# Kernel optimization log

Hardware: AMD Instinct MI355X
Metric: run time of the kernel (lower is better)

## Reference

```python
import jax, jax.numpy as jnp
import numpy as np

B, N, F_IN, H1, H2 = 32, 1024, 512, 256, 128


def _leaky(x, alpha):
    return jnp.where(x >= 0, x, alpha * x)


def _gat_layer(x, W, a, alpha=0.01, concat=True):
    # x: [B,N,Fin], W: [Fin,Fout], a: [2*Fout,1]
    h = x @ W                              # [B,N,Fout]
    Fo = W.shape[1]
    # The repeat+cat+matmul(a) in torch is exactly a_left . h_i + a_right . h_j
    el = h @ a[:Fo, 0]                     # [B,N]
    er = h @ a[Fo:, 0]                     # [B,N]
    e = _leaky(el[:, :, None] + er[:, None, :], alpha)   # [B,N,N]
    # global per-batch min-max normalization, then *30 - 20
    mn = jnp.min(e, axis=(1, 2), keepdims=True)
    mx = jnp.max(e, axis=(1, 2), keepdims=True)
    e = (e - mn) / (mx - mn) * 30.0 - 20.0
    att = jax.nn.sigmoid(e)                # [B,N,N]; dropout is a no-op in eval
    hp = att @ h                           # [B,N,Fout]
    if concat:
        hp = jax.nn.elu(hp)
    return hp, att


def setup_inputs() -> dict:
    key = jax.random.key(0)
    ks = jax.random.split(key, 8)
    x = jax.random.normal(ks[0], (B, N, F_IN), dtype=jnp.float32)
    edge_weight = jax.random.normal(ks[1], (B, N, N), dtype=jnp.float32)
    def xavier(k, shape):
        fan_in, fan_out = shape[0], shape[1]
        lim = 1.414 * np.sqrt(6.0 / (fan_in + fan_out))
        return jax.random.uniform(k, shape, jnp.float32, -lim, lim)
    W1 = xavier(ks[2], (F_IN, H1))
    a1 = xavier(ks[3], (2 * H1, 1))
    W2 = xavier(ks[4], (H1, H2))
    a2 = xavier(ks[5], (2 * H2, 1))
    Wg = jax.random.normal(ks[6], (H2, 1), dtype=jnp.float32) * np.sqrt(2.0 / H2)
    bg = jnp.zeros((1,), dtype=jnp.float32)
    return {"x": x, "edge_weight": edge_weight, "W1": W1, "a1": a1,
            "W2": W2, "a2": a2, "Wg": Wg, "bg": bg}


def reference(x, edge_weight, W1, a1, W2, a2, Wg, bg):
    # edge_weight ('adj') is never used inside GraphAttentionLayer.forward
    g1, fc1 = _gat_layer(x, W1, a1, alpha=0.01, concat=True)
    g2, fc2 = _gat_layer(g1, W2, a2, alpha=0.01, concat=False)
    # VanillaGCN: leaky_relu(BN(Linear(adj @ feats))); BN is identity in eval
    z = (fc2 @ g2) @ Wg + bg               # [B,N,1]
    out = _leaky(z, 0.01)
    return out, fc2, g2
```

## Files before the change

kernel.cpp:

```cpp
#include <hip/hip_runtime.h>

#define NN 1024
#define FIN 512
#define HH1 256
#define HH2 128
#define MTOT 32768

typedef unsigned short ushort_t;
using bf16x8 = __attribute__((ext_vector_type(8))) short;
using f32x4  = __attribute__((ext_vector_type(4))) float;

__device__ __forceinline__ float leakyf(float x) { return fmaxf(x, 0.01f * x); }
__device__ __forceinline__ float eluf(float x) { return x > 0.0f ? x : __expf(x) - 1.0f; }
__device__ __forceinline__ unsigned pack_hi(unsigned u0, unsigned u1) {
  return __builtin_amdgcn_perm(u1, u0, 0x07060302u);
}
__device__ __forceinline__ void split_pack2(float f0, float f1, unsigned& hp, unsigned& lp) {
  unsigned u0 = __float_as_uint(f0), u1 = __float_as_uint(f1);
  hp = pack_hi(u0, u1);
  float l0 = f0 - __uint_as_float(u0 & 0xFFFF0000u);
  float l1 = f1 - __uint_as_float(u1 & 0xFFFF0000u);
  lp = pack_hi(__float_as_uint(l0), __float_as_uint(l1));
}
__device__ __forceinline__ unsigned pack_rne(float f0, float f1) {
  unsigned u0 = __float_as_uint(f0); u0 += 0x7FFFu + ((u0 >> 16) & 1u);
  unsigned u1 = __float_as_uint(f1); u1 += 0x7FFFu + ((u1 >> 16) & 1u);
  return pack_hi(u0, u1);
}

__global__ __launch_bounds__(256) void transpose_w_split(const float* __restrict__ W,
                                                         ushort_t* __restrict__ WThi,
                                                         ushort_t* __restrict__ WTlo,
                                                         int Nc, int kshift) {
  int idx = blockIdx.x * 256 + threadIdx.x;
  int k = idx & ((1 << kshift) - 1);
  int n = idx >> kshift;
  float f = W[(size_t)k * Nc + n];
  unsigned u = __float_as_uint(f);
  WThi[idx] = (ushort_t)(u >> 16);
  float lo = f - __uint_as_float(u & 0xFFFF0000u);
  WTlo[idx] = (ushort_t)(__float_as_uint(lo) >> 16);
}

template<int NC>
__global__ __launch_bounds__(256) void gemm_asplit(const float* __restrict__ A,
                                                   const ushort_t* __restrict__ BThi,
                                                   const ushort_t* __restrict__ BTlo,
                                                   const float* __restrict__ avec,
                                                   ushort_t* __restrict__ CThi,
                                                   ushort_t* __restrict__ CTlo,
                                                   float* __restrict__ el,
                                                   float* __restrict__ er, int K) {
  constexpr int NFR = NC / 32;
  constexpr int NB  = NC / 64;
  __shared__ ushort_t Ah[64 * 40], Al[64 * 40];
  __shared__ ushort_t Bbuf[NC * 80];
  __shared__ float aL[NC], aR[NC];
  ushort_t* Bh = Bbuf;
  ushort_t* Bl = Bbuf + NC * 40;
  const int t = threadIdx.x, lane = t & 63, wid = t >> 6;
  const int wm = (wid & 1) * 32, wn = (wid >> 1) * (NC / 2);
  const int ln = lane & 15, quad = lane >> 4;
  const int m0 = blockIdx.x * 64;
  if (t < NC) { aL[t] = avec[t]; aR[t] = avec[NC + t]; }
  const int ra = t >> 2, ka = (t & 3) * 8;
  const float* ap = A + (size_t)(m0 + ra) * K + ka;
  const int brow = (t >> 2);
  const int bko  = (t & 3) * 8;
  f32x4 acc[2][NFR];
#pragma unroll
  for (int mi = 0; mi < 2; ++mi)
#pragma unroll
    for (int ni = 0; ni < NFR; ++ni) acc[mi][ni] = (f32x4){0.f, 0.f, 0.f, 0.f};

  for (int k0 = 0; k0 < K; k0 += 32) {
    float4 fa0 = *(const float4*)(ap + k0);
    float4 fa1 = *(const float4*)(ap + k0 + 4);
    uint4 vbh[NB], vbl[NB];
#pragma unroll
    for (int i = 0; i < NB; ++i) {
      size_t off = (size_t)(brow + i * 64) * K + k0 + bko;
      vbh[i] = *(const uint4*)&BThi[off];
      vbl[i] = *(const uint4*)&BTlo[off];
    }
    uint4 ah4, al4;
    split_pack2(fa0.x, fa0.y, ah4.x, al4.x);
    split_pack2(fa0.z, fa0.w, ah4.y, al4.y);
    split_pack2(fa1.x, fa1.y, ah4.z, al4.z);
    split_pack2(fa1.z, fa1.w, ah4.w, al4.w);
    __syncthreads();
    *(uint4*)&Ah[ra * 40 + ka] = ah4;
    *(uint4*)&Al[ra * 40 + ka] = al4;
#pragma unroll
    for (int i = 0; i < NB; ++i) {
      *(uint4*)&Bh[(brow + i * 64) * 40 + bko] = vbh[i];
      *(uint4*)&Bl[(brow + i * 64) * 40 + bko] = vbl[i];
    }
    __syncthreads();
    bf16x8 ahf[2], alf[2], bhf[NFR], blf[NFR];
#pragma unroll
    for (int i = 0; i < 2; ++i) {
      const int ao = (wm + i * 16 + ln) * 40 + quad * 8;
      ahf[i] = *(const bf16x8*)&Ah[ao];
      alf[i] = *(const bf16x8*)&Al[ao];
    }
#pragma unroll
    for (int i = 0; i < NFR; ++i) {
      const int bo = (wn + i * 16 + ln) * 40 + quad * 8;
      bhf[i] = *(const bf16x8*)&Bh[bo];
      blf[i] = *(const bf16x8*)&Bl[bo];
    }
#pragma unroll
    for (int mi = 0; mi < 2; ++mi)
#pragma unroll
      for (int ni = 0; ni < NFR; ++ni) {
        acc[mi][ni] = __builtin_amdgcn_mfma_f32_16x16x32_bf16(ahf[mi], bhf[ni], acc[mi][ni], 0, 0, 0);
        acc[mi][ni] = __builtin_amdgcn_mfma_f32_16x16x32_bf16(ahf[mi], blf[ni], acc[mi][ni], 0, 0, 0);
        acc[mi][ni] = __builtin_amdgcn_mfma_f32_16x16x32_bf16(alf[mi], bhf[ni], acc[mi][ni], 0, 0, 0);
      }
  }

#pragma unroll
  for (int mi = 0; mi < 2; ++mi) {
    const int mr = m0 + wm + mi * 16 + quad * 4;
#pragma unroll
    for (int rr = 0; rr < 4; ++rr) {
      float vel = 0.f, ver = 0.f;
#pragma unroll
      for (int ni = 0; ni < NFR; ++ni) {
        const int c = wn + ni * 16 + ln;
        vel = fmaf(acc[mi][ni][rr], aL[c], vel);
        ver = fmaf(acc[mi][ni][rr], aR[c], ver);
      }
#pragma unroll
      for (int m = 1; m < 16; m <<= 1) {
        vel += __shfl_xor(vel, m);
        ver += __shfl_xor(ver, m);
      }
      if (ln == 0) {
        atomicAdd(&el[mr + rr], vel);
        atomicAdd(&er[mr + rr], ver);
      }
    }
  }

  ushort_t* dsthi = CThi + (size_t)blockIdx.x * (NC * 64);
  ushort_t* dstlo = CTlo + (size_t)blockIdx.x * (NC * 64);
  const int colbase = wid * (NC / 4);
  const int g = lane >> 2, j = lane & 3;
#pragma unroll
  for (int pass = 0; pass < 2; ++pass) {
    __syncthreads();
#pragma unroll
    for (int mi = 0; mi < 2; ++mi) {
      const int rbase = wm + mi * 16 + quad * 4;
#pragma unroll
      for (int ni = 0; ni < NFR; ++ni) {
        const int c = wn + ni * 16 + ln;
        unsigned h01, l01, h23, l23;
        split_pack2(acc[mi][ni][0], acc[mi][ni][1], h01, l01);
        split_pack2(acc[mi][ni][2], acc[mi][ni][3], h23, l23);
        uint2 v = pass ? make_uint2(l01, l23) : make_uint2(h01, h23);
        *(uint2*)&Bbuf[c * 66 + rbase] = v;
      }
    }
    __syncthreads();
    ushort_t* dst = pass ? dstlo : dsthi;
#pragma unroll
    for (int cc = 0; cc < NC / 64; ++cc) {
      const int col = colbase + cc * 16 + g;
#pragma unroll
      for (int half = 0; half < 2; ++half) {
        const int r = half * 32 + j * 8;
        *(uint4*)&dst[col * 64 + r] = *(const uint4*)&Bbuf[col * 66 + r];
      }
    }
  }
}

__global__ __launch_bounds__(256) void minmax_params(const float* __restrict__ el,
                                                     const float* __restrict__ er,
                                                     float2* __restrict__ params) {
  __shared__ float smnl[256], smxl[256], smnr[256], smxr[256];
  const int b = blockIdx.x, t = threadIdx.x;
  float mnl = 3.4e38f, mxl = -3.4e38f, mnr = 3.4e38f, mxr = -3.4e38f;
  for (int i = t; i < NN; i += 256) {
    float v = el[b * NN + i];
    mnl = fminf(mnl, v); mxl = fmaxf(mxl, v);
    float u = er[b * NN + i];
    mnr = fminf(mnr, u); mxr = fmaxf(mxr, u);
  }
  smnl[t] = mnl; smxl[t] = mxl; smnr[t] = mnr; smxr[t] = mxr;
  __syncthreads();
  for (int s = 128; s > 0; s >>= 1) {
    if (t < s) {
      smnl[t] = fminf(smnl[t], smnl[t + s]);
      smxl[t] = fmaxf(smxl[t], smxl[t + s]);
      smnr[t] = fminf(smnr[t], smnr[t + s]);
      smxr[t] = fmaxf(smxr[t], smxr[t + s]);
    }
    __syncthreads();
  }
  if (t == 0) {
    float mn = leakyf(smnl[0] + smnr[0]);
    float mx = leakyf(smxl[0] + smxr[0]);
    params[b] = make_float2(mn, 30.0f / (mx - mn));
  }
}

__global__ __launch_bounds__(256) void gemm_att2(const float* __restrict__ el,
                                                 const float* __restrict__ er,
                                                 const float2* __restrict__ params,
                                                 const ushort_t* __restrict__ hThi,
                                                 const ushort_t* __restrict__ hTlo,
                                                 float* __restrict__ C,
                                                 const float* __restrict__ wg,
                                                 float* __restrict__ wv,
                                                 int Nc, int doElu) {
  __shared__ ushort_t Ah[64 * 40];
  __shared__ ushort_t Bh[128 * 40], Bl[128 * 40];
  __shared__ float ers[NN];
  __shared__ float wls[128];
  const int b = blockIdx.z, t = threadIdx.x, lane = t & 63, wid = t >> 6;
  const int wm = (wid & 1) * 32, wn = (wid >> 1) * 64;
  const int ln = lane & 15, quad = lane >> 4;
  const int m0 = blockIdx.x * 64, n0 = blockIdx.y * 128;
  const float2 p = params[b];
  const float npinv = -p.y;
  const float npc   = p.x * p.y + 20.0f;
  *(float4*)&ers[t * 4] = *(const float4*)&er[b * NN + t * 4];
  if (wg && t < 128) wls[t] = wg[t];
  const int ra = t >> 2, ka = (t & 3) * 8;
  const float elv = el[b * NN + m0 + ra];
  const int rb = t >> 1, kb = (t & 1) * 16;
  const size_t tstride = (size_t)Nc * 64;
  const size_t rowoff  = (size_t)(n0 + rb) * 64 + kb;
  f32x4 acc[2][4];
#pragma unroll
  for (int mi = 0; mi < 2; ++mi)
#pragma unroll
    for (int ni = 0; ni < 4; ++ni) acc[mi][ni] = (f32x4){0.f, 0.f, 0.f, 0.f};
  __syncthreads();

  for (int k0 = 0; k0 < NN; k0 += 32) {
    const size_t toff = (size_t)(b * 16 + (k0 >> 6)) * tstride + (size_t)(k0 & 32) + rowoff;
    uint4 vbh0 = *(const uint4*)&hThi[toff];
    uint4 vbh1 = *(const uint4*)&hThi[toff + 8];
    uint4 vbl0 = *(const uint4*)&hTlo[toff];
    uint4 vbl1 = *(const uint4*)&hTlo[toff + 8];
    float s[8];
#pragma unroll
    for (int j = 0; j < 8; ++j) {
      float x = elv + ers[k0 + ka + j];
      x = fmaxf(x, 0.01f * x);
      s[j] = __builtin_amdgcn_rcpf(1.0f + __expf(fmaf(x, npinv, npc)));
    }
    uint4 av;
    av.x = pack_rne(s[0], s[1]); av.y = pack_rne(s[2], s[3]);
    av.z = pack_rne(s[4], s[5]); av.w = pack_rne(s[6], s[7]);
    __syncthreads();
    *(uint4*)&Ah[ra * 40 + ka] = av;
    *(uint4*)&Bh[rb * 40 + kb] = vbh0; *(uint4*)&Bh[rb * 40 + kb + 8] = vbh1;
    *(uint4*)&Bl[rb * 40 + kb] = vbl0; *(uint4*)&Bl[rb * 40 + kb + 8] = vbl1;
    __syncthreads();
    bf16x8 af[2], bhf[4], blf[4];
#pragma unroll
    for (int i = 0; i < 2; ++i) af[i] = *(const bf16x8*)&Ah[(wm + i * 16 + ln) * 40 + quad * 8];
#pragma unroll
    for (int i = 0; i < 4; ++i) {
      const int bo = (wn + i * 16 + ln) * 40 + quad * 8;
      bhf[i] = *(const bf16x8*)&Bh[bo];
      blf[i] = *(const bf16x8*)&Bl[bo];
    }
#pragma unroll
    for (int mi = 0; mi < 2; ++mi)
#pragma unroll
      for (int ni = 0; ni < 4; ++ni) {
        acc[mi][ni] = __builtin_amdgcn_mfma_f32_16x16x32_bf16(af[mi], bhf[ni], acc[mi][ni], 0, 0, 0);
        acc[mi][ni] = __builtin_amdgcn_mfma_f32_16x16x32_bf16(af[mi], blf[ni], acc[mi][ni], 0, 0, 0);
      }
  }
#pragma unroll
  for (int mi = 0; mi < 2; ++mi) {
    const int mrl = m0 + wm + mi * 16 + quad * 4;
    const size_t mrow = (size_t)b * NN + mrl;
#pragma unroll
    for (int ni = 0; ni < 4; ++ni) {
      const int c = n0 + wn + ni * 16 + ln;
#pragma unroll
      for (int rr = 0; rr < 4; ++rr) {
        float v = acc[mi][ni][rr];
        if (doElu) v = eluf(v);
        C[(mrow + rr) * Nc + c] = v;
      }
    }
    if (wg) {
#pragma unroll
      for (int rr = 0; rr < 4; ++rr) {
        float vw = 0.f;
#pragma unroll
        for (int ni = 0; ni < 4; ++ni)
          vw = fmaf(acc[mi][ni][rr], wls[wn + ni * 16 + ln], vw);
#pragma unroll
        for (int m = 1; m < 16; m <<= 1) vw += __shfl_xor(vw, m);
        if (ln == 0) atomicAdd(&wv[b * NN + mrl + rr], vw);
      }
    }
  }
}

__global__ __launch_bounds__(256) void final_out_fc2(const float* __restrict__ el,
                                                     const float* __restrict__ er,
                                                     const float2* __restrict__ params,
                                                     const float* __restrict__ w,
                                                     const float* __restrict__ bg,
                                                     float* __restrict__ fc2,
                                                     float* __restrict__ out) {
  const int row  = (blockIdx.x * 256 + threadIdx.x) >> 6;
  const int lane = threadIdx.x & 63;
  const int b = row >> 10;
  const float2 p = params[b];
  const float npinv = -p.y;
  const float npc   = p.x * p.y + 20.0f;
  const float eli = el[row];
  const float* erb = er + (b << 10);
  const float* wb  = w + (b << 10);
  float* fcrow = fc2 + (size_t)row * NN;
  float s = 0.f;
  for (int j = lane * 4; j < NN; j += 256) {
    float4 e4 = *(const float4*)&erb[j];
    float4 w4 = *(const float4*)&wb[j];
    float4 a;
    a.x = __builtin_amdgcn_rcpf(1.0f + __expf(fmaf(leakyf(eli + e4.x), npinv, npc)));
    a.y = __builtin_amdgcn_rcpf(1.0f + __expf(fmaf(leakyf(eli + e4.y), npinv, npc)));
    a.z = __builtin_amdgcn_rcpf(1.0f + __expf(fmaf(leakyf(eli + e4.z), npinv, npc)));
    a.w = __builtin_amdgcn_rcpf(1.0f + __expf(fmaf(leakyf(eli + e4.w), npinv, npc)));
    s += w4.x * a.x + w4.y * a.y + w4.z * a.z + w4.w * a.w;
    *(float4*)&fcrow[j] = a;
  }
#pragma unroll
  for (int off = 32; off > 0; off >>= 1) s += __shfl_down(s, off);
  if (lane == 0) out[row] = leakyf(s + bg[0]);
}

extern "C" void kernel_launch(void* const* d_in, const int* in_sizes, int n_in,
                              void* d_out, int out_size, void* d_ws, size_t ws_size,
                              hipStream_t stream) {
  (void)in_sizes; (void)n_in; (void)out_size; (void)ws_size;
  const float* x  = (const float*)d_in[0];
  const float* W1 = (const float*)d_in[2];
  const float* a1 = (const float*)d_in[3];
  const float* W2 = (const float*)d_in[4];
  const float* a2 = (const float*)d_in[5];
  const float* Wg = (const float*)d_in[6];
  const float* bg = (const float*)d_in[7];

  float* out = (float*)d_out;
  float* fc2 = out + 32768;
  float* g2  = fc2 + 33554432;

  ushort_t* h1Thi = (ushort_t*)fc2;
  ushort_t* h1Tlo = (ushort_t*)(fc2 + 4194304);
  float*    g1    = fc2 + 8388608;
  ushort_t* h2Thi = (ushort_t*)(fc2 + 16777216);
  ushort_t* h2Tlo = (ushort_t*)(fc2 + 18874368);

  float* wsf = (float*)d_ws;
  float* el1 = wsf;
  float* er1 = wsf + 32768;
  float* el2 = wsf + 65536;
  float* er2 = wsf + 98304;
  float* wv  = wsf + 131072;
  float2* p1 = (float2*)(wsf + 163840);
  float2* p2 = (float2*)(wsf + 163904);
  ushort_t* W1Thi = (ushort_t*)(wsf + 163968);
  ushort_t* W1Tlo = (ushort_t*)(wsf + 229504);
  ushort_t* W2Thi = (ushort_t*)(wsf + 295040);
  ushort_t* W2Tlo = (ushort_t*)(wsf + 311424);

  dim3 blk(256);
  hipMemsetAsync(wsf, 0, 5u * 32768u * sizeof(float), stream);
  transpose_w_split<<<512, blk, 0, stream>>>(W1, W1Thi, W1Tlo, HH1, 9);
  transpose_w_split<<<128, blk, 0, stream>>>(W2, W2Thi, W2Tlo, HH2, 8);
  gemm_asplit<HH1><<<512, blk, 0, stream>>>(x, W1Thi, W1Tlo, a1,
                                            h1Thi, h1Tlo, el1, er1, FIN);
  minmax_params<<<32, blk, 0, stream>>>(el1, er1, p1);
  gemm_att2<<<dim3(16, 2, 32), blk, 0, stream>>>(el1, er1, p1, h1Thi, h1Tlo,
                                                 g1, nullptr, nullptr, HH1, 1);
  gemm_asplit<HH2><<<512, blk, 0, stream>>>(g1, W2Thi, W2Tlo, a2,
                                            h2Thi, h2Tlo, el2, er2, HH1);
  minmax_params<<<32, blk, 0, stream>>>(el2, er2, p2);
  gemm_att2<<<dim3(16, 1, 32), blk, 0, stream>>>(el2, er2, p2, h2Thi, h2Tlo,
                                                 g2, Wg, wv, HH2, 0);
  final_out_fc2<<<8192, blk, 0, stream>>>(el2, er2, p2, wv, bg, fc2, out);
}
```

Measured before the change: 498.8 us.

## Split GEMM column blocks across grid y to raise block count and occupancy

```diff
diff --git a/kernel.cpp b/kernel.cpp
--- a/kernel.cpp
+++ b/kernel.cpp
@@ -42,27 +42,28 @@
   WTlo[idx] = (ushort_t)(__float_as_uint(lo) >> 16);
 }
 
-template<int NC>
-__global__ __launch_bounds__(256) void gemm_asplit(const float* __restrict__ A,
-                                                   const ushort_t* __restrict__ BThi,
-                                                   const ushort_t* __restrict__ BTlo,
-                                                   const float* __restrict__ avec,
-                                                   ushort_t* __restrict__ CThi,
-                                                   ushort_t* __restrict__ CTlo,
-                                                   float* __restrict__ el,
-                                                   float* __restrict__ er, int K) {
-  constexpr int NFR = NC / 32;
-  constexpr int NB  = NC / 64;
+template<int NC, int NCB>
+__global__ __launch_bounds__(256, 4) void gemm_asplit(const float* __restrict__ A,
+                                                      const ushort_t* __restrict__ BThi,
+                                                      const ushort_t* __restrict__ BTlo,
+                                                      const float* __restrict__ avec,
+                                                      ushort_t* __restrict__ CThi,
+                                                      ushort_t* __restrict__ CTlo,
+                                                      float* __restrict__ el,
+                                                      float* __restrict__ er, int K) {
+  constexpr int NFR = NCB / 32;
+  constexpr int NB  = NCB / 64;
   __shared__ ushort_t Ah[64 * 40], Al[64 * 40];
-  __shared__ ushort_t Bbuf[NC * 80];
-  __shared__ float aL[NC], aR[NC];
+  __shared__ ushort_t Bbuf[NCB * 80];
+  __shared__ float aL[NCB], aR[NCB];
   ushort_t* Bh = Bbuf;
-  ushort_t* Bl = Bbuf + NC * 40;
+  ushort_t* Bl = Bbuf + NCB * 40;
   const int t = threadIdx.x, lane = t & 63, wid = t >> 6;
-  const int wm = (wid & 1) * 32, wn = (wid >> 1) * (NC / 2);
+  const int wm = (wid & 1) * 32, wn = (wid >> 1) * (NCB / 2);
   const int ln = lane & 15, quad = lane >> 4;
   const int m0 = blockIdx.x * 64;
-  if (t < NC) { aL[t] = avec[t]; aR[t] = avec[NC + t]; }
+  const int n0c = blockIdx.y * NCB;
+  if (t < NCB) { aL[t] = avec[n0c + t]; aR[t] = avec[NC + n0c + t]; }
   const int ra = t >> 2, ka = (t & 3) * 8;
   const float* ap = A + (size_t)(m0 + ra) * K + ka;
   const int brow = (t >> 2);
@@ -79,7 +80,7 @@
     uint4 vbh[NB], vbl[NB];
 #pragma unroll
     for (int i = 0; i < NB; ++i) {
-      size_t off = (size_t)(brow + i * 64) * K + k0 + bko;
+      size_t off = (size_t)(n0c + brow + i * 64) * K + k0 + bko;
       vbh[i] = *(const uint4*)&BThi[off];
       vbl[i] = *(const uint4*)&BTlo[off];
     }
@@ -144,9 +145,9 @@
     }
   }
 
-  ushort_t* dsthi = CThi + (size_t)blockIdx.x * (NC * 64);
-  ushort_t* dstlo = CTlo + (size_t)blockIdx.x * (NC * 64);
-  const int colbase = wid * (NC / 4);
+  ushort_t* dsthi = CThi + (size_t)blockIdx.x * (NC * 64) + (size_t)n0c * 64;
+  ushort_t* dstlo = CTlo + (size_t)blockIdx.x * (NC * 64) + (size_t)n0c * 64;
+  const int colbase = wid * (NCB / 4);
   const int g = lane >> 2, j = lane & 3;
 #pragma unroll
   for (int pass = 0; pass < 2; ++pass) {
@@ -167,7 +168,7 @@
     __syncthreads();
     ushort_t* dst = pass ? dstlo : dsthi;
 #pragma unroll
-    for (int cc = 0; cc < NC / 64; ++cc) {
+    for (int cc = 0; cc < NCB / 64; ++cc) {
       const int col = colbase + cc * 16 + g;
 #pragma unroll
       for (int half = 0; half < 2; ++half) {
@@ -208,46 +209,52 @@
   }
 }
 
-__global__ __launch_bounds__(256) void gemm_att2(const float* __restrict__ el,
-                                                 const float* __restrict__ er,
-                                                 const float2* __restrict__ params,
-                                                 const ushort_t* __restrict__ hThi,
-                                                 const ushort_t* __restrict__ hTlo,
-                                                 float* __restrict__ C,
-                                                 const float* __restrict__ wg,
-                                                 float* __restrict__ wv,
-                                                 int Nc, int doElu) {
+template<int BW>
+__global__ __launch_bounds__(256, 4) void gemm_att2(const float* __restrict__ el,
+                                                    const float* __restrict__ er,
+                                                    const float2* __restrict__ params,
+                                                    const ushort_t* __restrict__ hThi,
+                                                    const ushort_t* __restrict__ hTlo,
+                                                    float* __restrict__ C,
+                                                    const float* __restrict__ wg,
+                                                    float* __restrict__ wv,
+                                                    int Nc, int doElu) {
+  constexpr int NFR = BW / 32;
   __shared__ ushort_t Ah[64 * 40];
-  __shared__ ushort_t Bh[128 * 40], Bl[128 * 40];
+  __shared__ ushort_t Bh[BW * 40], Bl[BW * 40];
   __shared__ float ers[NN];
-  __shared__ float wls[128];
+  __shared__ float wls[BW];
   const int b = blockIdx.z, t = threadIdx.x, lane = t & 63, wid = t >> 6;
-  const int wm = (wid & 1) * 32, wn = (wid >> 1) * 64;
+  const int wm = (wid & 1) * 32, wn = (wid >> 1) * (BW / 2);
   const int ln = lane & 15, quad = lane >> 4;
-  const int m0 = blockIdx.x * 64, n0 = blockIdx.y * 128;
+  const int m0 = blockIdx.x * 64, n0 = blockIdx.y * BW;
   const float2 p = params[b];
   const float npinv = -p.y;
   const float npc   = p.x * p.y + 20.0f;
   *(float4*)&ers[t * 4] = *(const float4*)&er[b * NN + t * 4];
-  if (wg && t < 128) wls[t] = wg[t];
+  if (wg && t < BW) wls[t] = wg[n0 + t];
   const int ra = t >> 2, ka = (t & 3) * 8;
   const float elv = el[b * NN + m0 + ra];
-  const int rb = t >> 1, kb = (t & 1) * 16;
+  const int rb = (BW == 128) ? (t >> 1) : (t >> 2);
+  const int kb = (BW == 128) ? ((t & 1) * 16) : ((t & 3) * 8);
   const size_t tstride = (size_t)Nc * 64;
   const size_t rowoff  = (size_t)(n0 + rb) * 64 + kb;
-  f32x4 acc[2][4];
+  f32x4 acc[2][NFR];
 #pragma unroll
   for (int mi = 0; mi < 2; ++mi)
 #pragma unroll
-    for (int ni = 0; ni < 4; ++ni) acc[mi][ni] = (f32x4){0.f, 0.f, 0.f, 0.f};
+    for (int ni = 0; ni < NFR; ++ni) acc[mi][ni] = (f32x4){0.f, 0.f, 0.f, 0.f};
   __syncthreads();
 
   for (int k0 = 0; k0 < NN; k0 += 32) {
     const size_t toff = (size_t)(b * 16 + (k0 >> 6)) * tstride + (size_t)(k0 & 32) + rowoff;
     uint4 vbh0 = *(const uint4*)&hThi[toff];
-    uint4 vbh1 = *(const uint4*)&hThi[toff + 8];
     uint4 vbl0 = *(const uint4*)&hTlo[toff];
-    uint4 vbl1 = *(const uint4*)&hTlo[toff + 8];
+    uint4 vbh1, vbl1;
+    if constexpr (BW == 128) {
+      vbh1 = *(const uint4*)&hThi[toff + 8];
+      vbl1 = *(const uint4*)&hTlo[toff + 8];
+    }
     float s[8];
 #pragma unroll
     for (int j = 0; j < 8; ++j) {
@@ -260,14 +267,18 @@
     av.z = pack_rne(s[4], s[5]); av.w = pack_rne(s[6], s[7]);
     __syncthreads();
     *(uint4*)&Ah[ra * 40 + ka] = av;
-    *(uint4*)&Bh[rb * 40 + kb] = vbh0; *(uint4*)&Bh[rb * 40 + kb + 8] = vbh1;
-    *(uint4*)&Bl[rb * 40 + kb] = vbl0; *(uint4*)&Bl[rb * 40 + kb + 8] = vbl1;
-    __syncthreads();
-    bf16x8 af[2], bhf[4], blf[4];
+    *(uint4*)&Bh[rb * 40 + kb] = vbh0;
+    *(uint4*)&Bl[rb * 40 + kb] = vbl0;
+    if constexpr (BW == 128) {
+      *(uint4*)&Bh[rb * 40 + kb + 8] = vbh1;
+      *(uint4*)&Bl[rb * 40 + kb + 8] = vbl1;
+    }
+    __syncthreads();
+    bf16x8 af[2], bhf[NFR], blf[NFR];
 #pragma unroll
     for (int i = 0; i < 2; ++i) af[i] = *(const bf16x8*)&Ah[(wm + i * 16 + ln) * 40 + quad * 8];
 #pragma unroll
-    for (int i = 0; i < 4; ++i) {
+    for (int i = 0; i < NFR; ++i) {
       const int bo = (wn + i * 16 + ln) * 40 + quad * 8;
       bhf[i] = *(const bf16x8*)&Bh[bo];
       blf[i] = *(const bf16x8*)&Bl[bo];
@@ -275,7 +286,7 @@
 #pragma unroll
     for (int mi = 0; mi < 2; ++mi)
 #pragma unroll
-      for (int ni = 0; ni < 4; ++ni) {
+      for (int ni = 0; ni < NFR; ++ni) {
         acc[mi][ni] = __builtin_amdgcn_mfma_f32_16x16x32_bf16(af[mi], bhf[ni], acc[mi][ni], 0, 0, 0);
         acc[mi][ni] = __builtin_amdgcn_mfma_f32_16x16x32_bf16(af[mi], blf[ni], acc[mi][ni], 0, 0, 0);
       }
@@ -285,7 +296,7 @@
     const int mrl = m0 + wm + mi * 16 + quad * 4;
     const size_t mrow = (size_t)b * NN + mrl;
 #pragma unroll
-    for (int ni = 0; ni < 4; ++ni) {
+    for (int ni = 0; ni < NFR; ++ni) {
       const int c = n0 + wn + ni * 16 + ln;
 #pragma unroll
       for (int rr = 0; rr < 4; ++rr) {
@@ -299,7 +310,7 @@
       for (int rr = 0; rr < 4; ++rr) {
         float vw = 0.f;
 #pragma unroll
-        for (int ni = 0; ni < 4; ++ni)
+        for (int ni = 0; ni < NFR; ++ni)
           vw = fmaf(acc[mi][ni][rr], wls[wn + ni * 16 + ln], vw);
 #pragma unroll
         for (int m = 1; m < 16; m <<= 1) vw += __shfl_xor(vw, m);
@@ -382,15 +393,15 @@
   hipMemsetAsync(wsf, 0, 5u * 32768u * sizeof(float), stream);
   transpose_w_split<<<512, blk, 0, stream>>>(W1, W1Thi, W1Tlo, HH1, 9);
   transpose_w_split<<<128, blk, 0, stream>>>(W2, W2Thi, W2Tlo, HH2, 8);
-  gemm_asplit<HH1><<<512, blk, 0, stream>>>(x, W1Thi, W1Tlo, a1,
-                                            h1Thi, h1Tlo, el1, er1, FIN);
+  gemm_asplit<HH1, 128><<<dim3(512, 2), blk, 0, stream>>>(x, W1Thi, W1Tlo, a1,
+                                                          h1Thi, h1Tlo, el1, er1, FIN);
   minmax_params<<<32, blk, 0, stream>>>(el1, er1, p1);
-  gemm_att2<<<dim3(16, 2, 32), blk, 0, stream>>>(el1, er1, p1, h1Thi, h1Tlo,
-                                                 g1, nullptr, nullptr, HH1, 1);
-  gemm_asplit<HH2><<<512, blk, 0, stream>>>(g1, W2Thi, W2Tlo, a2,
-                                            h2Thi, h2Tlo, el2, er2, HH1);
+  gemm_att2<128><<<dim3(16, 2, 32), blk, 0, stream>>>(el1, er1, p1, h1Thi, h1Tlo,
+                                                      g1, nullptr, nullptr, HH1, 1);
+  gemm_asplit<HH2, 64><<<dim3(512, 2), blk, 0, stream>>>(g1, W2Thi, W2Tlo, a2,
+                                                         h2Thi, h2Tlo, el2, er2, HH1);
   minmax_params<<<32, blk, 0, stream>>>(el2, er2, p2);
-  gemm_att2<<<dim3(16, 1, 32), blk, 0, stream>>>(el2, er2, p2, h2Thi, h2Tlo,
-                                                 g2, Wg, wv, HH2, 0);
+  gemm_att2<64><<<dim3(16, 2, 32), blk, 0, stream>>>(el2, er2, p2, h2Thi, h2Tlo,
+                                                     g2, Wg, wv, HH2, 0);
   final_out_fc2<<<8192, blk, 0, stream>>>(el2, er2, p2, wv, bg, fc2, out);
 }
```

New measurement: 484.8 us. 1.03x faster.
